# Kernel optimization log

Hardware: AMD Instinct MI355X
Metric: run time of the kernel (lower is better)

The kernel has to match this reference:

```python
import jax, jax.numpy as jnp
import numpy as np

B, S, E = 2, 2048, 2048
H, D = 16, 128           # n_heads, head_dim (= rope_dim)
BASE = 10000.0


def _rope_tables(seq_len, dim):
    inv_freq = 1.0 / (BASE ** (jnp.arange(0, dim, 2, dtype=jnp.float32) / dim))
    t = jnp.arange(seq_len, dtype=jnp.float32)
    freqs = jnp.outer(t, inv_freq)                 # [S, D/2]
    emb = jnp.concatenate([freqs, freqs], axis=-1)  # [S, D]
    cos = jnp.cos(emb)[None, :, None, :]            # [1, S, 1, D]
    sin = jnp.sin(emb)[None, :, None, :]
    return cos, sin


def _rotate_half(x):
    x1, x2 = x[..., : x.shape[-1] // 2], x[..., x.shape[-1] // 2:]
    return jnp.concatenate([-x2, x1], axis=-1)


def setup_inputs() -> dict:
    key = jax.random.key(0)
    ks = jax.random.split(key, 9)
    s = 1.0 / np.sqrt(E)
    return {
        "x": jax.random.normal(ks[0], (B, S, E), dtype=jnp.float32),
        "Wq": jax.random.uniform(ks[1], (E, E), jnp.float32, -s, s),
        "bq": jax.random.uniform(ks[2], (E,), jnp.float32, -s, s),
        "Wk": jax.random.uniform(ks[3], (E, E), jnp.float32, -s, s),
        "bk": jax.random.uniform(ks[4], (E,), jnp.float32, -s, s),
        "Wv": jax.random.uniform(ks[5], (E, E), jnp.float32, -s, s),
        "bv": jax.random.uniform(ks[6], (E,), jnp.float32, -s, s),
        "Wp": jax.random.uniform(ks[7], (E, E), jnp.float32, -s, s),
        "bp": jax.random.uniform(ks[8], (E,), jnp.float32, -s, s),
    }


def reference(x, Wq, bq, Wk, bk, Wv, bv, Wp, bp):
    b, s, e = x.shape
    # QKV projections (torch Linear: y = x W^T + b)
    q = (jnp.einsum("bse,fe->bsf", x, Wq) + bq).reshape(b, s, H, D)
    k = (jnp.einsum("bse,fe->bsf", x, Wk) + bk).reshape(b, s, H, D)
    v = (jnp.einsum("bse,fe->bsf", x, Wv) + bv).reshape(b, s, H, D)
    # RoPE (rope_dim == head_dim, start_pos = 0)
    cos, sin = _rope_tables(s, D)
    q = q * cos + _rotate_half(q) * sin
    k = k * cos + _rotate_half(k) * sin
    # attention scores [b, m, n, h]
    att = jnp.einsum("bmhd,bnhd->bmnh", q, k)
    causal = jnp.tril(jnp.ones((s, s), dtype=bool))[None, :, :, None]
    att = jnp.where(causal, att, -jnp.inf)
    att = jax.nn.softmax(att / np.sqrt(D), axis=2)
    out = jnp.einsum("bmnh,bnhd->bmhd", att, v).reshape(b, s, e)
    return jnp.einsum("bse,fe->bsf", out, Wp) + bp
```

## Files before the change

kernel.cpp:

```cpp
#include <hip/hip_runtime.h>
#include <hip/hip_bf16.h>
#include <math.h>

#define BB 2
#define SS 2048
#define EE 2048
#define HH 16
#define DD 128
#define MM (BB*SS)

typedef __attribute__((ext_vector_type(8))) short bf16x8;
typedef __attribute__((ext_vector_type(4))) float f32x4;

__device__ inline float bf2f(const __hip_bfloat16 h){ return __bfloat162float(h); }
__device__ inline __hip_bfloat16 f2bf(float f){ return __float2bfloat16(f); }
__device__ inline short f2bs(float f){
  union { __hip_bfloat16 h; short s; } u; u.h = __float2bfloat16(f); return u.s;
}

__device__ inline void gload16(const void* g, void* l){
  __builtin_amdgcn_global_load_lds((const __attribute__((address_space(1))) void*)g,
      (__attribute__((address_space(3))) void*)l, 16, 0, 0);
}

__global__ void cvt_kernel(const float* __restrict__ in, __hip_bfloat16* __restrict__ out, int n4){
  int i = blockIdx.x*256 + threadIdx.x;
  if (i >= n4) return;
  float4 v = ((const float4*)in)[i];
  union { short4 s4; short s[4]; } u;
  u.s[0] = f2bs(v.x); u.s[1] = f2bs(v.y); u.s[2] = f2bs(v.z); u.s[3] = f2bs(v.w);
  ((short4*)out)[i] = u.s4;
}

struct P4 { const float* s0; const float* s1; const float* s2; const float* s3;
            __hip_bfloat16* d0; __hip_bfloat16* d1; __hip_bfloat16* d2; __hip_bfloat16* d3; };
__global__ void cvt4_kernel(P4 p, int n4){
  int w = blockIdx.y;
  const float* in = w==0 ? p.s0 : w==1 ? p.s1 : w==2 ? p.s2 : p.s3;
  __hip_bfloat16* out = w==0 ? p.d0 : w==1 ? p.d1 : w==2 ? p.d2 : p.d3;
  int i = blockIdx.x*256 + threadIdx.x;
  if (i >= n4) return;
  float4 v = ((const float4*)in)[i];
  union { short4 s4; short s[4]; } u;
  u.s[0] = f2bs(v.x); u.s[1] = f2bs(v.y); u.s[2] = f2bs(v.z); u.s[3] = f2bs(v.w);
  ((short4*)out)[i] = u.s4;
}

__global__ void rope_tables_kernel(float* __restrict__ cost, float* __restrict__ sint){
  int idx = blockIdx.x*256 + threadIdx.x;
  int s = idx >> 6, i = idx & 63;
  double inv = exp(-log(10000.0) * (double)i / 64.0);
  double f = (double)s * inv;
  cost[idx] = (float)cos(f);
  sint[idx] = (float)sin(f);
}

__global__ void rope_kernel(__hip_bfloat16* __restrict__ q, __hip_bfloat16* __restrict__ k,
                            const float* __restrict__ cost, const float* __restrict__ sint){
  int idx = blockIdx.x*256 + threadIdx.x;
  int i = idx & 63;
  int h = (idx >> 6) & (HH-1);
  int bs = idx >> 10;
  int s = bs & (SS-1);
  float c = cost[s*64 + i], sn = sint[s*64 + i];
  size_t base = ((size_t)bs*HH + h)*DD + i;
  float q1 = bf2f(q[base]), q2 = bf2f(q[base+64]);
  q[base]    = f2bf(q1*c - q2*sn);
  q[base+64] = f2bf(q2*c + q1*sn);
  float k1 = bf2f(k[base]), k2 = bf2f(k[base+64]);
  k[base]    = f2bf(k1*c - k2*sn);
  k[base+64] = f2bf(k2*c + k1*sn);
}

template<int MODE>
__global__ __launch_bounds__(512) void gemm256(const __hip_bfloat16* __restrict__ A,
        const __hip_bfloat16* __restrict__ Bw, const float* __restrict__ bias,
        void* __restrict__ Cout){
  __shared__ __align__(1024) char lds[98304];
  const int tid = threadIdx.x, wid = tid>>6, lane = tid&63, g = lane>>4, c16 = lane&15;
  const int wm = wid>>2, wn = wid&3;
  const int orig = blockIdx.x;
  const int wg = (orig & 7)*32 + (orig >> 3);
  const int bm = wg & 31, bn = wg >> 5;
  const int rowA0 = bm*128, rowB0 = bn*256;
  const char* Ab8 = (const char*)A + (size_t)rowA0*4096;
  const char* Bb8 = (const char*)Bw + (size_t)rowB0*4096;

  f32x4 acc[4][4] = {};

  auto stage = [&](int t, int b){
    char* ad = lds + b*49152;
    char* bd = lds + b*49152 + 16384;
    #pragma unroll
    for (int i=0;i<2;i++){
      int off = i*8192 + tid*16;
      int r = off >> 7;
      int cs = (off & 127) ^ ((r&7)<<4);
      gload16(Ab8 + (size_t)r*4096 + t*128 + cs, ad + i*8192 + wid*1024);
    }
    #pragma unroll
    for (int i=0;i<4;i++){
      int off = i*8192 + tid*16;
      int r = off >> 7;
      int cs = (off & 127) ^ ((r&7)<<4);
      gload16(Bb8 + (size_t)r*4096 + t*128 + cs, bd + i*8192 + wid*1024);
    }
  };

  auto compute = [&](int b){
    const char* Abuf = lds + b*49152;
    const char* Bbuf = lds + b*49152 + 16384;
    bf16x8 bfr[4][2];
    #pragma unroll
    for (int ni=0;ni<4;ni++){
      int r = wn*64 + ni*16 + c16;
      int sw = (r&7)<<4;
      #pragma unroll
      for (int kk=0;kk<2;kk++)
        bfr[ni][kk] = *(const bf16x8*)(Bbuf + r*128 + ((kk*64 + g*16) ^ sw));
    }
    #pragma unroll
    for (int mi=0;mi<4;mi++){
      int r = wm*64 + mi*16 + c16;
      int sw = (r&7)<<4;
      bf16x8 af0 = *(const bf16x8*)(Abuf + r*128 + ((g*16) ^ sw));
      bf16x8 af1 = *(const bf16x8*)(Abuf + r*128 + ((64 + g*16) ^ sw));
      __builtin_amdgcn_s_setprio(1);
      #pragma unroll
      for (int ni=0;ni<4;ni++){
        acc[mi][ni] = __builtin_amdgcn_mfma_f32_16x16x32_bf16(af0, bfr[ni][0], acc[mi][ni],0,0,0);
        acc[mi][ni] = __builtin_amdgcn_mfma_f32_16x16x32_bf16(af1, bfr[ni][1], acc[mi][ni],0,0,0);
      }
      __builtin_amdgcn_s_setprio(0);
    }
  };

  stage(0,0);
  stage(1,1);
  asm volatile("s_waitcnt vmcnt(6)" ::: "memory");
  asm volatile("s_barrier" ::: "memory");

  #pragma unroll 1
  for (int tt = 0; tt < 32; tt += 2){
    compute(0);
    asm volatile("s_barrier" ::: "memory");
    if (tt + 2 < 32){ stage(tt+2, 0); asm volatile("s_waitcnt vmcnt(6)" ::: "memory"); }
    else            {                 asm volatile("s_waitcnt vmcnt(0)" ::: "memory"); }
    asm volatile("s_barrier" ::: "memory");
    compute(1);
    if (tt + 2 < 32){
      asm volatile("s_barrier" ::: "memory");
      if (tt + 3 < 32){ stage(tt+3, 1); asm volatile("s_waitcnt vmcnt(6)" ::: "memory"); }
      else            {                 asm volatile("s_waitcnt vmcnt(0)" ::: "memory"); }
      asm volatile("s_barrier" ::: "memory");
    }
  }

  #pragma unroll
  for (int mi=0;mi<4;mi++){
    #pragma unroll
    for (int ni=0;ni<4;ni++){
      int f = rowB0 + wn*64 + ni*16 + c16;
      float bv = bias[f];
      #pragma unroll
      for (int j=0;j<4;j++){
        int m = rowA0 + wm*64 + mi*16 + g*4 + j;
        float v = acc[mi][ni][j] + bv;
        if constexpr (MODE == 0) {
          ((__hip_bfloat16*)Cout)[(size_t)m*EE + f] = f2bf(v);
        } else if constexpr (MODE == 1) {
          int b = m >> 11, s = m & (SS-1);
          ((__hip_bfloat16*)Cout)[((size_t)(b*EE + f))*SS + s] = f2bf(v);
        } else {
          ((float*)Cout)[(size_t)m*EE + f] = v;
        }
      }
    }
  }
}

__global__ __launch_bounds__(256) void attn_kernel(const __hip_bfloat16* __restrict__ qg,
    const __hip_bfloat16* __restrict__ kg, const __hip_bfloat16* __restrict__ vtg,
    __hip_bfloat16* __restrict__ og){
  __shared__ short Ks[2][64*128];
  __shared__ short Vs[2][128*64];
  __shared__ short Pl[4][16*76];
  const int tid=threadIdx.x, wid=tid>>6, lane=tid&63, g=lane>>4, c16=lane&15;
  const int bq = blockIdx.x, bh = blockIdx.y, b = bh>>4, h = bh&15;
  const char* kb8 = (const char*)(kg + ((size_t)b*SS)*EE + h*DD);
  const char* vb8 = (const char*)(vtg + (size_t)bh*DD*SS);
  const __hip_bfloat16* qbase = qg + ((size_t)b*SS)*EE + h*DD;
  const float SCL = 0.08838834764831845f * 1.4426950408889634f;

  #pragma unroll 1
  for (int t = 0; t < 2; ++t){
    const int qtile = t ? bq : (31 - bq);
    const int q0 = qtile*64, qw = q0 + wid*16;
    const int niter = qtile + 1;

    bf16x8 qf[4];
    #pragma unroll
    for (int ds=0; ds<4; ds++)
      qf[ds] = *(const bf16x8*)&qbase[(size_t)(qw + c16)*EE + ds*32 + g*8];

    f32x4 oacc[8] = {};
    float mrun[4], lrun[4];
    #pragma unroll
    for (int j=0;j<4;j++){ mrun[j] = -INFINITY; lrun[j] = 0.f; }

    #pragma unroll
    for (int i=0;i<4;i++){
      int base = i*4096 + wid*1024;
      int lb = base + lane*16;
      int r = lb >> 8, cb = lb & 255;
      gload16(kb8 + (size_t)r*4096 + (cb ^ ((r&7)<<4)), (char*)Ks[0] + base);
    }
    #pragma unroll
    for (int i=0;i<4;i++){
      int base = i*4096 + wid*1024;
      int lb = base + lane*16;
      int d = lb >> 7, cb = lb & 127;
      gload16(vb8 + (size_t)d*4096 + (cb ^ ((d&7)<<4)), (char*)Vs[0] + base);
    }
    __syncthreads();

    int cur = 0;
    #pragma unroll 1
    for (int it = 0; it < niter; ++it){
      const int kv0 = it*64;
      if (it + 1 < niter){
        const int kn = kv0 + 64;
        #pragma unroll
        for (int i=0;i<4;i++){
          int base = i*4096 + wid*1024;
          int lb = base + lane*16;
          int r = lb >> 8, cb = lb & 255;
          gload16(kb8 + (size_t)(kn + r)*4096 + (cb ^ ((r&7)<<4)), (char*)Ks[cur^1] + base);
        }
        #pragma unroll
        for (int i=0;i<4;i++){
          int base = i*4096 + wid*1024;
          int lb = base + lane*16;
          int d = lb >> 7, cb = lb & 127;
          gload16(vb8 + (size_t)d*4096 + (size_t)kn*2 + (cb ^ ((d&7)<<4)), (char*)Vs[cur^1] + base);
        }
      }

      f32x4 sacc[4] = {};
      #pragma unroll
      for (int kq=0; kq<4; kq++){
        int row = kq*16 + c16;
        int rsw = (c16 & 7) << 4;
        #pragma unroll
        for (int ds=0; ds<4; ds++){
          bf16x8 kf = *(const bf16x8*)((const char*)Ks[cur] + row*256 + ((ds*64 + g*16) ^ rsw));
          sacc[kq] = __builtin_amdgcn_mfma_f32_16x16x32_bf16(qf[ds], kf, sacc[kq], 0,0,0);
        }
      }

      if (kv0 + 63 > qw){
        #pragma unroll
        for (int kq=0; kq<4; kq++)
          #pragma unroll
          for (int j=0;j<4;j++)
            if (kv0 + kq*16 + c16 > qw + g*4 + j) sacc[kq][j] = -INFINITY;
      }

      float pr[4][4], rs[4];
      #pragma unroll
      for (int j=0;j<4;j++){
        float m = fmaxf(fmaxf(sacc[0][j], sacc[1][j]), fmaxf(sacc[2][j], sacc[3][j]));
        #pragma unroll
        for (int off=8; off>=1; off>>=1) m = fmaxf(m, __shfl_xor(m, off, 16));
        float mnew = fmaxf(mrun[j], m);
        rs[j] = exp2f((mrun[j] - mnew)*SCL);
        mrun[j] = mnew;
        float ps = 0.f;
        #pragma unroll
        for (int kq=0; kq<4; kq++){
          pr[kq][j] = exp2f((sacc[kq][j] - mnew)*SCL);
          ps += pr[kq][j];
        }
        #pragma unroll
        for (int off=8; off>=1; off>>=1) ps += __shfl_xor(ps, off, 16);
        lrun[j] = lrun[j]*rs[j] + ps;
      }
      #pragma unroll
      for (int dc=0; dc<8; dc++){
        f32x4 o = oacc[dc];
        o[0]*=rs[0]; o[1]*=rs[1]; o[2]*=rs[2]; o[3]*=rs[3];
        oacc[dc] = o;
      }

      #pragma unroll
      for (int j=0;j<4;j++)
        #pragma unroll
        for (int kq=0; kq<4; kq++)
          Pl[wid][(g*4+j)*76 + kq*16 + c16] = f2bs(pr[kq][j]);
      bf16x8 pf[2];
      #pragma unroll
      for (int kc=0; kc<2; kc++)
        pf[kc] = *(const bf16x8*)&Pl[wid][c16*76 + kc*32 + g*8];

      #pragma unroll
      for (int dc=0; dc<8; dc++){
        int row = dc*16 + c16;
        int rsw = (c16 & 7) << 4;
        #pragma unroll
        for (int kc=0; kc<2; kc++){
          bf16x8 vf = *(const bf16x8*)((const char*)Vs[cur] + row*128 + ((kc*64 + g*16) ^ rsw));
          oacc[dc] = __builtin_amdgcn_mfma_f32_16x16x32_bf16(pf[kc], vf, oacc[dc], 0,0,0);
        }
      }

      __syncthreads();
      cur ^= 1;
    }

    float inv[4];
    #pragma unroll
    for (int j=0;j<4;j++) inv[j] = 1.0f / lrun[j];
    #pragma unroll
    for (int dc=0; dc<8; dc++)
      #pragma unroll
      for (int j=0;j<4;j++)
        og[((size_t)(b*SS + qw + g*4 + j))*EE + h*DD + dc*16 + c16] = f2bf(oacc[dc][j]*inv[j]);
    __syncthreads();
  }
}

extern "C" void kernel_launch(void* const* d_in, const int* in_sizes, int n_in,
                              void* d_out, int out_size, void* d_ws, size_t ws_size,
                              hipStream_t stream){
  const float* x  = (const float*)d_in[0];
  const float* Wq = (const float*)d_in[1];
  const float* bq = (const float*)d_in[2];
  const float* Wk = (const float*)d_in[3];
  const float* bk = (const float*)d_in[4];
  const float* Wv = (const float*)d_in[5];
  const float* bv = (const float*)d_in[6];
  const float* Wp = (const float*)d_in[7];
  const float* bp = (const float*)d_in[8];
  float* out = (float*)d_out;

  char* ws = (char*)d_ws;
  size_t off = 0;
  auto alloc = [&](size_t bytes){ void* p = ws + off; off += (bytes + 255) & ~(size_t)255; return p; };
  const size_t nx = (size_t)MM*EE;
  const size_t nw = (size_t)EE*EE;
  __hip_bfloat16* xb  = (__hip_bfloat16*)alloc(nx*2);
  __hip_bfloat16* wqb = (__hip_bfloat16*)alloc(nw*2);
  __hip_bfloat16* wkb = (__hip_bfloat16*)alloc(nw*2);
  __hip_bfloat16* wvb = (__hip_bfloat16*)alloc(nw*2);
  __hip_bfloat16* wpb = (__hip_bfloat16*)alloc(nw*2);
  __hip_bfloat16* qb  = (__hip_bfloat16*)alloc(nx*2);
  __hip_bfloat16* kb  = (__hip_bfloat16*)alloc(nx*2);
  __hip_bfloat16* vtb = (__hip_bfloat16*)alloc(nx*2);
  __hip_bfloat16* ob  = (__hip_bfloat16*)alloc(nx*2);
  float* cost = (float*)alloc((size_t)SS*64*4);
  float* sint = (float*)alloc((size_t)SS*64*4);

  cvt_kernel<<<(int)(nx/4/256), 256, 0, stream>>>(x, xb, (int)(nx/4));
  P4 p4{Wq, Wk, Wv, Wp, wqb, wkb, wvb, wpb};
  cvt4_kernel<<<dim3((int)(nw/4/256), 4), 256, 0, stream>>>(p4, (int)(nw/4));
  rope_tables_kernel<<<SS*64/256, 256, 0, stream>>>(cost, sint);

  gemm256<0><<<256, 512, 0, stream>>>(xb, wqb, bq, qb);
  gemm256<0><<<256, 512, 0, stream>>>(xb, wkb, bk, kb);
  gemm256<1><<<256, 512, 0, stream>>>(xb, wvb, bv, vtb);

  rope_kernel<<<(BB*SS*HH*64)/256, 256, 0, stream>>>(qb, kb, cost, sint);

  attn_kernel<<<dim3(16, BB*HH), 256, 0, stream>>>(qb, kb, vtb, ob);

  gemm256<2><<<256, 512, 0, stream>>>(ob, wpb, bp, out);
}
```

Baseline: 303.5 us.

## Rework attention to 32x32 MFMA with transposed scores and register-resident P

Restructures the flash-attention kernel to use 32x32x16 MFMA tiles, computing S^T so each lane owns one query row. This removes the 16-lane shuffle reductions and the LDS round-trip for P, which is now repacked in registers via cross-half shuffles. The grid changes from 16x32 blocks that each process two paired 64-row tiles to 512 blocks of 128-row tiles, ordered heavy-first for load balance, with launch bounds requesting 2 blocks per CU. Register pressure from 64 accumulator floats per lane plus 32 P values may limit occupancy.

```diff
diff --git a/kernel.cpp b/kernel.cpp
--- a/kernel.cpp
+++ b/kernel.cpp
@@ -11,11 +11,17 @@
 
 typedef __attribute__((ext_vector_type(8))) short bf16x8;
 typedef __attribute__((ext_vector_type(4))) float f32x4;
+typedef __attribute__((ext_vector_type(16))) float f32x16;
+typedef __attribute__((ext_vector_type(4))) unsigned u32x4;
 
 __device__ inline float bf2f(const __hip_bfloat16 h){ return __bfloat162float(h); }
 __device__ inline __hip_bfloat16 f2bf(float f){ return __float2bfloat16(f); }
 __device__ inline short f2bs(float f){
   union { __hip_bfloat16 h; short s; } u; u.h = __float2bfloat16(f); return u.s;
+}
+__device__ inline unsigned pk2(float a, float b){
+  union { __hip_bfloat162 h2; unsigned u; } x;
+  x.h2 = __float22bfloat162_rn(float2{a,b}); return x.u;
 }
 
 __device__ inline void gload16(const void* g, void* l){
@@ -179,153 +185,166 @@
   }
 }
 
-__global__ __launch_bounds__(256) void attn_kernel(const __hip_bfloat16* __restrict__ qg,
+__global__ __launch_bounds__(256, 2) void attn_kernel(const __hip_bfloat16* __restrict__ qg,
     const __hip_bfloat16* __restrict__ kg, const __hip_bfloat16* __restrict__ vtg,
     __hip_bfloat16* __restrict__ og){
   __shared__ short Ks[2][64*128];
   __shared__ short Vs[2][128*64];
-  __shared__ short Pl[4][16*76];
-  const int tid=threadIdx.x, wid=tid>>6, lane=tid&63, g=lane>>4, c16=lane&15;
-  const int bq = blockIdx.x, bh = blockIdx.y, b = bh>>4, h = bh&15;
+  const int tid=threadIdx.x, wid=tid>>6, lane=tid&63;
+  const int c32 = lane & 31, hi = lane >> 5;
+  const int id = blockIdx.x;
+  const int u = id & 255;
+  const int bh = u & 31, pr = u >> 5;
+  const int qtile = (id < 256) ? (15 - pr) : pr;
+  const int b = bh >> 4, h = bh & 15;
+  const int q0 = qtile*128, qw = q0 + wid*32;
+  const int qglob = qw + c32;
+  const int niter = 2*qtile + 2;
+
   const char* kb8 = (const char*)(kg + ((size_t)b*SS)*EE + h*DD);
   const char* vb8 = (const char*)(vtg + (size_t)bh*DD*SS);
-  const __hip_bfloat16* qbase = qg + ((size_t)b*SS)*EE + h*DD;
   const float SCL = 0.08838834764831845f * 1.4426950408889634f;
 
-  #pragma unroll 1
-  for (int t = 0; t < 2; ++t){
-    const int qtile = t ? bq : (31 - bq);
-    const int q0 = qtile*64, qw = q0 + wid*16;
-    const int niter = qtile + 1;
-
-    bf16x8 qf[4];
-    #pragma unroll
-    for (int ds=0; ds<4; ds++)
-      qf[ds] = *(const bf16x8*)&qbase[(size_t)(qw + c16)*EE + ds*32 + g*8];
-
-    f32x4 oacc[8] = {};
-    float mrun[4], lrun[4];
-    #pragma unroll
-    for (int j=0;j<4;j++){ mrun[j] = -INFINITY; lrun[j] = 0.f; }
-
+  const char* qrow = (const char*)(qg + ((size_t)(b*SS + qglob))*EE + h*DD);
+  bf16x8 qf[8];
+  #pragma unroll
+  for (int s=0;s<8;s++) qf[s] = *(const bf16x8*)(qrow + s*32 + hi*16);
+
+  f32x16 pacc[4] = {};
+  float mrun = -INFINITY, lrun = 0.f;
+
+  auto stageK = [&](int kv, int buf){
     #pragma unroll
     for (int i=0;i<4;i++){
       int base = i*4096 + wid*1024;
       int lb = base + lane*16;
       int r = lb >> 8, cb = lb & 255;
-      gload16(kb8 + (size_t)r*4096 + (cb ^ ((r&7)<<4)), (char*)Ks[0] + base);
-    }
+      gload16(kb8 + (size_t)(kv + r)*4096 + (cb ^ ((r&7)<<4)), (char*)Ks[buf] + base);
+    }
+  };
+  auto stageV = [&](int kv, int buf){
     #pragma unroll
     for (int i=0;i<4;i++){
       int base = i*4096 + wid*1024;
       int lb = base + lane*16;
       int d = lb >> 7, cb = lb & 127;
-      gload16(vb8 + (size_t)d*4096 + (cb ^ ((d&7)<<4)), (char*)Vs[0] + base);
-    }
+      gload16(vb8 + (size_t)d*4096 + (size_t)kv*2 + (cb ^ ((d&7)<<4)), (char*)Vs[buf] + base);
+    }
+  };
+
+  stageK(0,0); stageV(0,0);
+  __syncthreads();
+
+  int cur = 0;
+  #pragma unroll 1
+  for (int it = 0; it < niter; ++it){
+    const int kv0 = it*64;
+    if (it + 1 < niter){ stageK(kv0+64, cur^1); stageV(kv0+64, cur^1); }
+
+    f32x16 st0 = {}, st1 = {};
+    {
+      const char* Kb = (const char*)Ks[cur];
+      const int sw = (c32 & 7) << 4;
+      #pragma unroll
+      for (int s=0;s<8;s++){
+        bf16x8 kf0 = *(const bf16x8*)(Kb + c32*256        + ((s*32 + hi*16) ^ sw));
+        bf16x8 kf1 = *(const bf16x8*)(Kb + (32+c32)*256   + ((s*32 + hi*16) ^ sw));
+        st0 = __builtin_amdgcn_mfma_f32_32x32x16_bf16(kf0, qf[s], st0, 0,0,0);
+        st1 = __builtin_amdgcn_mfma_f32_32x32x16_bf16(kf1, qf[s], st1, 0,0,0);
+      }
+    }
+
+    float p[32];
+    float vmax = -INFINITY;
+    const bool domask = (kv0 + 63 > qw);
+    #pragma unroll
+    for (int r=0;r<16;r++){
+      float v0 = st0[r], v1 = st1[r];
+      if (domask){
+        int kvo = (r&3) + 8*(r>>2) + 4*hi;
+        if (kv0 + kvo > qglob)      v0 = -INFINITY;
+        if (kv0 + 32 + kvo > qglob) v1 = -INFINITY;
+      }
+      p[r] = v0; p[16+r] = v1;
+      vmax = fmaxf(vmax, fmaxf(v0, v1));
+    }
+    vmax = fmaxf(vmax, __shfl_xor(vmax, 32));
+    const float mnew = fmaxf(mrun, vmax);
+    const float rs = exp2f((mrun - mnew)*SCL);
+    mrun = mnew;
+    float ps = 0.f;
+    #pragma unroll
+    for (int i=0;i<32;i++){
+      p[i] = exp2f((p[i] - mnew)*SCL);
+      ps += p[i];
+    }
+    ps += __shfl_xor(ps, 32);
+    lrun = lrun*rs + ps;
+
+    #pragma unroll
+    for (int ds=0; ds<4; ds++)
+      #pragma unroll
+      for (int r=0;r<16;r++) pacc[ds][r] *= rs;
+
+    unsigned w[2][4][2];
+    #pragma unroll
+    for (int T=0;T<2;T++)
+      #pragma unroll
+      for (int m=0;m<4;m++)
+        #pragma unroll
+        for (int uu=0;uu<2;uu++)
+          w[T][m][uu] = pk2(p[T*16 + 4*m + 2*uu], p[T*16 + 4*m + 2*uu + 1]);
+
+    bf16x8 pf[4];
+    #pragma unroll
+    for (int ks=0; ks<4; ks++){
+      int T = ks>>1, lo2 = (ks&1)*2;
+      unsigned o0 = hi ? w[T][lo2+1][0] : w[T][lo2+0][0];
+      unsigned o1 = hi ? w[T][lo2+1][1] : w[T][lo2+0][1];
+      unsigned s0 = hi ? w[T][lo2+0][0] : w[T][lo2+1][0];
+      unsigned s1 = hi ? w[T][lo2+0][1] : w[T][lo2+1][1];
+      unsigned r0 = (unsigned)__shfl_xor((int)s0, 32);
+      unsigned r1 = (unsigned)__shfl_xor((int)s1, 32);
+      union { u32x4 u4; bf16x8 h8; } cvt;
+      cvt.u4[0] = hi ? r0 : o0;
+      cvt.u4[1] = hi ? r1 : o1;
+      cvt.u4[2] = hi ? o0 : r0;
+      cvt.u4[3] = hi ? o1 : r1;
+      pf[ks] = cvt.h8;
+    }
+
+    {
+      const char* Vb = (const char*)Vs[cur];
+      const int vsw = (c32 & 7) << 4;
+      #pragma unroll
+      for (int ds=0; ds<4; ds++){
+        const char* vr = Vb + (ds*32 + c32)*128;
+        #pragma unroll
+        for (int ks=0; ks<4; ks++){
+          bf16x8 vf = *(const bf16x8*)(vr + ((ks*32 + hi*16) ^ vsw));
+          pacc[ds] = __builtin_amdgcn_mfma_f32_32x32x16_bf16(vf, pf[ks], pacc[ds], 0,0,0);
+        }
+      }
+    }
+
     __syncthreads();
-
-    int cur = 0;
-    #pragma unroll 1
-    for (int it = 0; it < niter; ++it){
-      const int kv0 = it*64;
-      if (it + 1 < niter){
-        const int kn = kv0 + 64;
-        #pragma unroll
-        for (int i=0;i<4;i++){
-          int base = i*4096 + wid*1024;
-          int lb = base + lane*16;
-          int r = lb >> 8, cb = lb & 255;
-          gload16(kb8 + (size_t)(kn + r)*4096 + (cb ^ ((r&7)<<4)), (char*)Ks[cur^1] + base);
-        }
-        #pragma unroll
-        for (int i=0;i<4;i++){
-          int base = i*4096 + wid*1024;
-          int lb = base + lane*16;
-          int d = lb >> 7, cb = lb & 127;
-          gload16(vb8 + (size_t)d*4096 + (size_t)kn*2 + (cb ^ ((d&7)<<4)), (char*)Vs[cur^1] + base);
-        }
-      }
-
-      f32x4 sacc[4] = {};
-      #pragma unroll
-      for (int kq=0; kq<4; kq++){
-        int row = kq*16 + c16;
-        int rsw = (c16 & 7) << 4;
-        #pragma unroll
-        for (int ds=0; ds<4; ds++){
-          bf16x8 kf = *(const bf16x8*)((const char*)Ks[cur] + row*256 + ((ds*64 + g*16) ^ rsw));
-          sacc[kq] = __builtin_amdgcn_mfma_f32_16x16x32_bf16(qf[ds], kf, sacc[kq], 0,0,0);
-        }
-      }
-
-      if (kv0 + 63 > qw){
-        #pragma unroll
-        for (int kq=0; kq<4; kq++)
-          #pragma unroll
-          for (int j=0;j<4;j++)
-            if (kv0 + kq*16 + c16 > qw + g*4 + j) sacc[kq][j] = -INFINITY;
-      }
-
-      float pr[4][4], rs[4];
-      #pragma unroll
-      for (int j=0;j<4;j++){
-        float m = fmaxf(fmaxf(sacc[0][j], sacc[1][j]), fmaxf(sacc[2][j], sacc[3][j]));
-        #pragma unroll
-        for (int off=8; off>=1; off>>=1) m = fmaxf(m, __shfl_xor(m, off, 16));
-        float mnew = fmaxf(mrun[j], m);
-        rs[j] = exp2f((mrun[j] - mnew)*SCL);
-        mrun[j] = mnew;
-        float ps = 0.f;
-        #pragma unroll
-        for (int kq=0; kq<4; kq++){
-          pr[kq][j] = exp2f((sacc[kq][j] - mnew)*SCL);
-          ps += pr[kq][j];
-        }
-        #pragma unroll
-        for (int off=8; off>=1; off>>=1) ps += __shfl_xor(ps, off, 16);
-        lrun[j] = lrun[j]*rs[j] + ps;
-      }
-      #pragma unroll
-      for (int dc=0; dc<8; dc++){
-        f32x4 o = oacc[dc];
-        o[0]*=rs[0]; o[1]*=rs[1]; o[2]*=rs[2]; o[3]*=rs[3];
-        oacc[dc] = o;
-      }
-
-      #pragma unroll
-      for (int j=0;j<4;j++)
-        #pragma unroll
-        for (int kq=0; kq<4; kq++)
-          Pl[wid][(g*4+j)*76 + kq*16 + c16] = f2bs(pr[kq][j]);
-      bf16x8 pf[2];
-      #pragma unroll
-      for (int kc=0; kc<2; kc++)
-        pf[kc] = *(const bf16x8*)&Pl[wid][c16*76 + kc*32 + g*8];
-
-      #pragma unroll
-      for (int dc=0; dc<8; dc++){
-        int row = dc*16 + c16;
-        int rsw = (c16 & 7) << 4;
-        #pragma unroll
-        for (int kc=0; kc<2; kc++){
-          bf16x8 vf = *(const bf16x8*)((const char*)Vs[cur] + row*128 + ((kc*64 + g*16) ^ rsw));
-          oacc[dc] = __builtin_amdgcn_mfma_f32_16x16x32_bf16(pf[kc], vf, oacc[dc], 0,0,0);
-        }
-      }
-
-      __syncthreads();
-      cur ^= 1;
-    }
-
-    float inv[4];
-    #pragma unroll
-    for (int j=0;j<4;j++) inv[j] = 1.0f / lrun[j];
-    #pragma unroll
-    for (int dc=0; dc<8; dc++)
-      #pragma unroll
-      for (int j=0;j<4;j++)
-        og[((size_t)(b*SS + qw + g*4 + j))*EE + h*DD + dc*16 + c16] = f2bf(oacc[dc][j]*inv[j]);
-    __syncthreads();
+    cur ^= 1;
+  }
+
+  const float invl = 1.0f / lrun;
+  char* orow = (char*)(og + ((size_t)(b*SS + qglob))*EE + h*DD);
+  #pragma unroll
+  for (int ds=0; ds<4; ds++){
+    #pragma unroll
+    for (int m=0;m<4;m++){
+      int d0 = ds*32 + 8*m + 4*hi;
+      short4 s4;
+      s4.x = f2bs(pacc[ds][4*m+0]*invl);
+      s4.y = f2bs(pacc[ds][4*m+1]*invl);
+      s4.z = f2bs(pacc[ds][4*m+2]*invl);
+      s4.w = f2bs(pacc[ds][4*m+3]*invl);
+      *(short4*)(orow + d0*2) = s4;
+    }
   }
 }
 
@@ -371,7 +390,7 @@
 
   rope_kernel<<<(BB*SS*HH*64)/256, 256, 0, stream>>>(qb, kb, cost, sint);
 
-  attn_kernel<<<dim3(16, BB*HH), 256, 0, stream>>>(qb, kb, vtb, ob);
+  attn_kernel<<<dim3(512), 256, 0, stream>>>(qb, kb, vtb, ob);
 
   gemm256<2><<<256, 512, 0, stream>>>(ob, wpb, bp, out);
 }
```

New measurement: 284.6 us. 6.3% less time.
